# Kernel optimization log

Hardware: AMD Instinct MI355X
Metric: run time of the kernel (lower is better)

## Reference

```python
import jax, jax.numpy as jnp
import numpy as np

N_APP = 100000
N_ATTR = 50000
E = 500000
D_IN = 128
D_H = 128
D_OUT = 2


def _sage(h_src, h_dst, src, dst, ew, W_self, W_neigh, b, n_dst):
    # DGL SAGEConv('mean') with edge_weight: m_e = ew_e * h_src[src_e];
    # h_neigh_v = sum_e->v m_e / in_degree(v); out = h_dst@W_self + h_neigh@W_neigh + b
    # (feat_drop=0.2 is identity in eval mode)
    m = h_src[src] * ew[:, None]                                   # [E, d]
    s = jax.ops.segment_sum(m, dst, num_segments=n_dst)            # [n_dst, d]
    deg = jax.ops.segment_sum(jnp.ones_like(ew), dst, num_segments=n_dst)
    h_neigh = s / jnp.maximum(deg, 1.0)[:, None]
    return h_dst @ W_self + h_neigh @ W_neigh + b


def _forward(x_app, x_attr, ew0, ew1, ew2,
             Wself1, Wneigh1, b1, Wself2, Wneigh2, b2, Wc, bc,
             src0, dst0, src1, dst1, src2, dst2):
    # ---- layer 1 (HeteroGraphConv, aggregate='sum' over relations per dst ntype) ----
    h_attr = _sage(x_app, x_attr, src0, dst0, ew0, Wself1[0], Wneigh1[0], b1[0], N_ATTR)
    h_app = (_sage(x_attr, x_app, src1, dst1, ew1, Wself1[1], Wneigh1[1], b1[1], N_APP)
             + _sage(x_app, x_app, src2, dst2, ew2, Wself1[2], Wneigh1[2], b1[2], N_APP))
    h_attr = jax.nn.relu(h_attr)
    h_app = jax.nn.relu(h_app)
    # ---- layer 2 ----
    h_attr2 = _sage(h_app, h_attr, src0, dst0, ew0, Wself2[0], Wneigh2[0], b2[0], N_ATTR)
    h_app2 = (_sage(h_attr, h_app, src1, dst1, ew1, Wself2[1], Wneigh2[1], b2[1], N_APP)
              + _sage(h_app, h_app, src2, dst2, ew2, Wself2[2], Wneigh2[2], b2[2], N_APP))
    del h_attr2  # second layer output on 'attribute' is unused by classify
    # ---- classify on 'application' ----
    return h_app2 @ Wc + bc


def setup_inputs() -> dict:
    key = jax.random.key(0)
    ks = jax.random.split(key, 20)
    sc = 1.0 / np.sqrt(D_H)
    return {
        "x_app": jax.random.normal(ks[0], (N_APP, D_IN), jnp.float32),
        "x_attr": jax.random.normal(ks[1], (N_ATTR, D_IN), jnp.float32),
        "ew0": jax.random.uniform(ks[2], (E,), jnp.float32),
        "ew1": jax.random.uniform(ks[3], (E,), jnp.float32),
        "ew2": jax.random.uniform(ks[4], (E,), jnp.float32),
        "Wself1": jax.random.normal(ks[5], (3, D_IN, D_H), jnp.float32) * sc,
        "Wneigh1": jax.random.normal(ks[6], (3, D_IN, D_H), jnp.float32) * sc,
        "b1": jax.random.normal(ks[7], (3, D_H), jnp.float32) * 0.01,
        "Wself2": jax.random.normal(ks[8], (3, D_H, D_H), jnp.float32) * sc,
        "Wneigh2": jax.random.normal(ks[9], (3, D_H, D_H), jnp.float32) * sc,
        "b2": jax.random.normal(ks[10], (3, D_H), jnp.float32) * 0.01,
        "Wc": jax.random.normal(ks[11], (D_H, D_OUT), jnp.float32) * sc,
        "bc": jax.random.normal(ks[12], (D_OUT,), jnp.float32) * 0.01,
        "src0": jax.random.randint(ks[13], (E,), 0, N_APP, jnp.int32),
        "dst0": jax.random.randint(ks[14], (E,), 0, N_ATTR, jnp.int32),
        "src1": jax.random.randint(ks[15], (E,), 0, N_ATTR, jnp.int32),
        "dst1": jax.random.randint(ks[16], (E,), 0, N_APP, jnp.int32),
        "src2": jax.random.randint(ks[17], (E,), 0, N_APP, jnp.int32),
        "dst2": jax.random.randint(ks[18], (E,), 0, N_APP, jnp.int32),
    }


def reference(x_app, x_attr, ew0, ew1, ew2,
              Wself1, Wneigh1, b1, Wself2, Wneigh2, b2, Wc, bc,
              src0, dst0, src1, dst1, src2, dst2):
    return _forward(x_app, x_attr, ew0, ew1, ew2,
                    Wself1, Wneigh1, b1, Wself2, Wneigh2, b2, Wc, bc,
                    src0, dst0, src1, dst1, src2, dst2)
```

## Files before the change

kernel.cpp:

```cpp
#include <hip/hip_runtime.h>

#define NAPP  100000
#define NATTR 50000
#define NE    500000
#define D     128
#define NTOT  (NATTR + 2 * NAPP)
#define SCHUNK 1024
#define SNB   ((NTOT + SCHUNK - 1) / SCHUNK)
#define EGRID ((NE + 255) / 256)
#define GB_APP  ((NAPP + 63) / 64)
#define GB_ATTR ((NATTR + 63) / 64)

typedef __attribute__((ext_vector_type(8))) short bfrag;
typedef __attribute__((ext_vector_type(4))) float f32x4;

__device__ __forceinline__ short bf16_rn(float x) {
    union { float f; unsigned u; } a; a.f = x;
    unsigned r = (a.u + 0x7fffu + ((a.u >> 16) & 1u)) >> 16;
    return (short)r;
}
__device__ __forceinline__ float bf16_to_f(short s) {
    union { float f; unsigned u; } a;
    a.u = ((unsigned)(unsigned short)s) << 16;
    return a.f;
}

__device__ __forceinline__ void split2(float x, float y, unsigned& hw, unsigned& lw) {
    union { float f; unsigned u; } ax, ay;
    ax.f = x; ay.f = y;
    unsigned hx = (ax.u + 0x7fffu + ((ax.u >> 16) & 1u)) >> 16;
    unsigned hy = (ay.u + 0x7fffu + ((ay.u >> 16) & 1u)) >> 16;
    union { unsigned u; float f; } fx, fy;
    fx.u = hx << 16; fy.u = hy << 16;
    union { float f; unsigned u; } rx, ry;
    rx.f = x - fx.f; ry.f = y - fy.f;
    unsigned lx = (rx.u + 0x7fffu + ((rx.u >> 16) & 1u)) >> 16;
    unsigned ly = (ry.u + 0x7fffu + ((ry.u >> 16) & 1u)) >> 16;
    hw = (hy << 16) | (hx & 0xffffu);
    lw = (ly << 16) | (lx & 0xffffu);
}

__global__ __launch_bounds__(256) void hist3_kernel(
        const int* __restrict__ d0, const int* __restrict__ d1, const int* __restrict__ d2,
        int* __restrict__ h0, int* __restrict__ h1, int* __restrict__ h2) {
    int b = blockIdx.x;
    int rel = b / EGRID;
    int i = (b - rel * EGRID) * 256 + threadIdx.x;
    if (i >= NE) return;
    const int* dst = (rel == 0) ? d0 : (rel == 1) ? d1 : d2;
    int* h = (rel == 0) ? h0 : (rel == 1) ? h1 : h2;
    atomicAdd(&h[dst[i]], 1);
}

__global__ __launch_bounds__(256) void scan_partial_kernel(const int* __restrict__ cur,
                                                           int* __restrict__ bsum) {
    int b = blockIdx.x, t = threadIdx.x;
    int4 v = *((const int4*)(cur + b * SCHUNK) + t);
    int s = v.x + v.y + v.z + v.w;
    __shared__ int sd[256];
    sd[t] = s;
    __syncthreads();
    for (int off = 128; off > 0; off >>= 1) {
        if (t < off) sd[t] += sd[t + off];
        __syncthreads();
    }
    if (t == 0) bsum[b] = sd[0];
}

__global__ __launch_bounds__(256) void scan_offsets_kernel(const int* __restrict__ bsum,
        int* __restrict__ boff, int* __restrict__ rp0, int* __restrict__ rp1,
        int* __restrict__ rp2) {
    int t = threadIdx.x;
    int v = (t < SNB) ? bsum[t] : 0;
    __shared__ int sd[256];
    sd[t] = v;
    __syncthreads();
    for (int off = 1; off < 256; off <<= 1) {
        int u = (t >= off) ? sd[t - off] : 0;
        __syncthreads();
        sd[t] += u;
        __syncthreads();
    }
    boff[t] = sd[t] - v;
    if (t == 0) { rp0[NATTR] = NE; rp1[NAPP] = NE; rp2[NAPP] = NE; }
}

__global__ __launch_bounds__(256) void scan_final_kernel(int* __restrict__ cur,
        const int* __restrict__ boff, int* __restrict__ rp0, int* __restrict__ rp1,
        int* __restrict__ rp2) {
    int b = blockIdx.x, t = threadIdx.x;
    int base = b * SCHUNK + t * 4;
    int4 v = *(const int4*)(cur + base);
    int s = v.x + v.y + v.z + v.w;
    __shared__ int sd[256];
    sd[t] = s;
    __syncthreads();
    for (int off = 1; off < 256; off <<= 1) {
        int u = (t >= off) ? sd[t - off] : 0;
        __syncthreads();
        sd[t] += u;
        __syncthreads();
    }
    int pre = boff[b] + sd[t] - s;
    int ex[4];
    ex[0] = pre;
    ex[1] = ex[0] + v.x;
    ex[2] = ex[1] + v.y;
    ex[3] = ex[2] + v.z;
    #pragma unroll
    for (int i = 0; i < 4; i++) {
        int idx = base + i;
        if (idx < NTOT) {
            int* rp; int loc; int rbase;
            if (idx < NATTR)             { rp = rp0; loc = idx;                 rbase = 0; }
            else if (idx < NATTR + NAPP) { rp = rp1; loc = idx - NATTR;        rbase = NE; }
            else                         { rp = rp2; loc = idx - NATTR - NAPP; rbase = 2 * NE; }
            int val = ex[i] - rbase;
            rp[loc] = val;
            cur[idx] = val;
        }
    }
}

__global__ __launch_bounds__(256) void scatter3_kernel(
        const int* __restrict__ s0, const int* __restrict__ d0, const float* __restrict__ e0,
        int* __restrict__ c0, int2* __restrict__ cw0,
        const int* __restrict__ s1, const int* __restrict__ d1, const float* __restrict__ e1,
        int* __restrict__ c1, int2* __restrict__ cw1,
        const int* __restrict__ s2, const int* __restrict__ d2, const float* __restrict__ e2,
        int* __restrict__ c2, int2* __restrict__ cw2) {
    int b = blockIdx.x;
    int rel = b / EGRID;
    int i = (b - rel * EGRID) * 256 + threadIdx.x;
    if (i >= NE) return;
    const int* src; const int* dst; const float* ew; int* cur; int2* cw;
    if (rel == 0)      { src = s0; dst = d0; ew = e0; cur = c0; cw = cw0; }
    else if (rel == 1) { src = s1; dst = d1; ew = e1; cur = c1; cw = cw1; }
    else               { src = s2; dst = d2; ew = e2; cur = c2; cw = cw2; }
    int p = atomicAdd(&cur[dst[i]], 1);
    int2 v;
    v.x = src[i];
    v.y = __float_as_int(ew[i]);
    cw[p] = v;
}

__global__ __launch_bounds__(256) void pack_kernel(
        const float* __restrict__ Wself1, const float* __restrict__ Wneigh1,
        const float* __restrict__ Wself2, const float* __restrict__ Wneigh2,
        const float* __restrict__ b1, const float* __restrict__ b2,
        const float* __restrict__ Wc, const float* __restrict__ bc,
        short* __restrict__ PBh, short* __restrict__ PBl,
        float* __restrict__ b1s, float* __restrict__ b2s,
        float* __restrict__ Cs, float* __restrict__ C1, float* __restrict__ C2,
        float* __restrict__ bconst) {
    int m = blockIdx.x;
    if (m == 8) {
        int tid = threadIdx.x;
        int k = tid >> 1, j = tid & 1;
        const float* Wn1 = Wneigh2 + D * D;
        const float* Wn2 = Wneigh2 + 2 * D * D;
        const float* Ws1 = Wself2 + D * D;
        const float* Ws2 = Wself2 + 2 * D * D;
        float ss = 0.f, s1 = 0.f, s2 = 0.f;
        for (int tt = 0; tt < D; tt++) {
            float wc = Wc[tt * 2 + j];
            ss += (Ws1[k * D + tt] + Ws2[k * D + tt]) * wc;
            s1 += Wn1[k * D + tt] * wc;
            s2 += Wn2[k * D + tt] * wc;
        }
        Cs[tid] = ss; C1[tid] = s1; C2[tid] = s2;
        if (tid < 2) {
            float s = bc[tid];
            for (int tt = 0; tt < D; tt++)
                s += (b2[D + tt] + b2[2 * D + tt]) * Wc[tt * 2 + tid];
            bconst[tid] = s;
        }
        return;
    }
    const float* srcA; const float* srcB = nullptr;
    switch (m) {
        case 0: srcA = Wself1; break;
        case 1: srcA = Wneigh1; break;
        case 2: srcA = Wself1 + D * D; srcB = Wself1 + 2 * D * D; break;
        case 3: srcA = Wneigh1 + D * D; break;
        case 4: srcA = Wneigh1 + 2 * D * D; break;
        case 5: srcA = Wself2 + D * D; srcB = Wself2 + 2 * D * D; break;
        case 6: srcA = Wneigh2 + D * D; break;
        default: srcA = Wneigh2 + 2 * D * D; break;
    }
    short* oh = PBh + (size_t)m * D * D;
    short* ol = PBl + (size_t)m * D * D;
    for (int i = threadIdx.x; i < D * D; i += 256) {
        int k = i >> 7, n = i & 127;
        float v = srcA[i];
        if (srcB) v += srcB[i];
        short hi = bf16_rn(v);
        short lo = bf16_rn(v - bf16_to_f(hi));
        int kc = k >> 5, q = (k >> 3) & 3, j = k & 7, nt = n >> 4, c = n & 15;
        int pos = (((kc * 8 + nt) * 64) + q * 16 + c) * 8 + j;
        oh[pos] = hi;
        ol[pos] = lo;
    }
    if (m == 0 && threadIdx.x < D) {
        int t = threadIdx.x;
        b1s[t] = b1[D + t] + b1[2 * D + t];
        b2s[t] = b2[D + t] + b2[2 * D + t];
    }
}

#define ASTR 128
template<int NG>
__device__ __forceinline__ void fused_body(
        const float* __restrict__ in0, const short* __restrict__ B0h, const short* __restrict__ B0l,
        const float* __restrict__ x1, const int* __restrict__ rp1, const int2* __restrict__ cw1,
        const short* __restrict__ B1h, const short* __restrict__ B1l,
        const float* __restrict__ x2, const int* __restrict__ rp2, const int2* __restrict__ cw2,
        const short* __restrict__ B2h, const short* __restrict__ B2l,
        const float* __restrict__ bias,
        const float* __restrict__ Ccol0, const float* __restrict__ Ccol1,
        float* __restrict__ zo0, float* __restrict__ zo1,
        int nrows, int row0, float* At) {
    const int t = threadIdx.x;
    const int w = t >> 6, lane = t & 63;
    const int q = lane >> 4, c = lane & 15;
    const int myrow = row0 + w * 16 + c;
    const int arow = min(myrow, nrows - 1);

    f32x4 acc[8];
    #pragma unroll
    for (int nt = 0; nt < 8; nt++) acc[nt] = (f32x4){0.f, 0.f, 0.f, 0.f};

    {
        const float* __restrict__ arp = in0 + (size_t)arow * D;
        const bfrag* __restrict__ Bh = (const bfrag*)B0h;
        const bfrag* __restrict__ Bl = (const bfrag*)B0l;
        #pragma unroll
        for (int kc = 0; kc < 4; kc++) {
            float4 a0 = *(const float4*)(arp + kc * 32 + q * 8);
            float4 a1 = *(const float4*)(arp + kc * 32 + q * 8 + 4);
            union { unsigned u[4]; bfrag v; } ahu, alu;
            split2(a0.x, a0.y, ahu.u[0], alu.u[0]);
            split2(a0.z, a0.w, ahu.u[1], alu.u[1]);
            split2(a1.x, a1.y, ahu.u[2], alu.u[2]);
            split2(a1.z, a1.w, ahu.u[3], alu.u[3]);
            bfrag ah = ahu.v, al = alu.v;
            const bfrag* bh = Bh + kc * 512 + lane;
            const bfrag* bl = Bl + kc * 512 + lane;
            #pragma unroll
            for (int nt = 0; nt < 8; nt++) {
                bfrag vh = bh[nt * 64];
                bfrag vl = bl[nt * 64];
                acc[nt] = __builtin_amdgcn_mfma_f32_16x16x32_bf16(ah, vh, acc[nt], 0, 0, 0);
                acc[nt] = __builtin_amdgcn_mfma_f32_16x16x32_bf16(ah, vl, acc[nt], 0, 0, 0);
                acc[nt] = __builtin_amdgcn_mfma_f32_16x16x32_bf16(al, vh, acc[nt], 0, 0, 0);
            }
        }
    }

    const int grp = t >> 5, l32 = t & 31;
    #pragma unroll
    for (int g = 0; g < NG; g++) {
        const float* __restrict__ xs = (g == 0) ? x1 : x2;
        const int* __restrict__ rp   = (g == 0) ? rp1 : rp2;
        const int2* __restrict__ cw  = (g == 0) ? cw1 : cw2;
        const short* __restrict__ Bhp = (g == 0) ? B1h : B2h;
        const short* __restrict__ Blp = (g == 0) ? B1l : B2l;

        if (g > 0) __syncthreads();
        {
            const int r0g = row0 + grp * 8;
            int bnd[9];
            #pragma unroll
            for (int i = 0; i < 9; i++) bnd[i] = rp[min(r0g + i, nrows)];
            #pragma unroll
            for (int p = 0; p < 4; p++) {
                const int A0 = bnd[2 * p],     A1 = bnd[2 * p + 1];
                const int B0 = bnd[2 * p + 1], B1 = bnd[2 * p + 2];
                float4 aA = make_float4(0.f, 0.f, 0.f, 0.f);
                float4 aB = make_float4(0.f, 0.f, 0.f, 0.f);
                const int lastA = min(max(A1 - 1, A0), NE - 1);
                const int lastB = min(max(B1 - 1, B0), NE - 1);
                int jA = A0, jB = B0;
                while (jA < A1 || jB < B1) {
                    int2 ed[8];
                    #pragma unroll
                    for (int u = 0; u < 4; u++) ed[u] = cw[min(jA + u, lastA)];
                    #pragma unroll
                    for (int u = 0; u < 4; u++) ed[4 + u] = cw[min(jB + u, lastB)];
                    float wt[8];
                    #pragma unroll
                    for (int u = 0; u < 4; u++)
                        wt[u] = (jA + u < A1) ? __int_as_float(ed[u].y) : 0.f;
                    #pragma unroll
                    for (int u = 0; u < 4; u++)
                        wt[4 + u] = (jB + u < B1) ? __int_as_float(ed[4 + u].y) : 0.f;
                    float4 v[8];
                    #pragma unroll
                    for (int u = 0; u < 8; u++)
                        v[u] = *(const float4*)(xs + (size_t)ed[u].x * D + l32 * 4);
                    aA.x += wt[0] * v[0].x + wt[1] * v[1].x + wt[2] * v[2].x + wt[3] * v[3].x;
                    aA.y += wt[0] * v[0].y + wt[1] * v[1].y + wt[2] * v[2].y + wt[3] * v[3].y;
                    aA.z += wt[0] * v[0].z + wt[1] * v[1].z + wt[2] * v[2].z + wt[3] * v[3].z;
                    aA.w += wt[0] * v[0].w + wt[1] * v[1].w + wt[2] * v[2].w + wt[3] * v[3].w;
                    aB.x += wt[4] * v[4].x + wt[5] * v[5].x + wt[6] * v[6].x + wt[7] * v[7].x;
                    aB.y += wt[4] * v[4].y + wt[5] * v[5].y + wt[6] * v[6].y + wt[7] * v[7].y;
                    aB.z += wt[4] * v[4].z + wt[5] * v[5].z + wt[6] * v[6].z + wt[7] * v[7].z;
                    aB.w += wt[4] * v[4].w + wt[5] * v[5].w + wt[6] * v[6].w + wt[7] * v[7].w;
                    jA += 4; jB += 4;
                }
                const float invA = 1.0f / (float)max(A1 - A0, 1);
                const float invB = 1.0f / (float)max(B1 - B0, 1);
                aA.x *= invA; aA.y *= invA; aA.z *= invA; aA.w *= invA;
                aB.x *= invB; aB.y *= invB; aB.z *= invB; aB.w *= invB;
                const int lrA = grp * 8 + 2 * p;
                const int lrB = lrA + 1;
                *(float4*)&At[lrA * ASTR + ((l32 ^ ((lrA & 3) << 1)) << 2)] = aA;
                *(float4*)&At[lrB * ASTR + ((l32 ^ ((lrB & 3) << 1)) << 2)] = aB;
            }
        }
        __syncthreads();

        const bfrag* __restrict__ Bh = (const bfrag*)Bhp;
        const bfrag* __restrict__ Bl = (const bfrag*)Blp;
        const int rloc = w * 16 + c;
        const int sw = (rloc & 3) << 1;
        const float* __restrict__ arow_lds = &At[rloc * ASTR];
        #pragma unroll
        for (int kc = 0; kc < 4; kc++) {
            const int g0 = kc * 8 + q * 2;
            float4 a0 = *(const float4*)(arow_lds + ((g0 ^ sw) << 2));
            float4 a1 = *(const float4*)(arow_lds + (((g0 + 1) ^ sw) << 2));
            union { unsigned u[4]; bfrag v; } ahu, alu;
            split2(a0.x, a0.y, ahu.u[0], alu.u[0]);
            split2(a0.z, a0.w, ahu.u[1], alu.u[1]);
            split2(a1.x, a1.y, ahu.u[2], alu.u[2]);
            split2(a1.z, a1.w, ahu.u[3], alu.u[3]);
            bfrag ah = ahu.v, al = alu.v;
            const bfrag* bh = Bh + kc * 512 + lane;
            const bfrag* bl = Bl + kc * 512 + lane;
            #pragma unroll
            for (int nt = 0; nt < 8; nt++) {
                bfrag vh = bh[nt * 64];
                bfrag vl = bl[nt * 64];
                acc[nt] = __builtin_amdgcn_mfma_f32_16x16x32_bf16(ah, vh, acc[nt], 0, 0, 0);
                acc[nt] = __builtin_amdgcn_mfma_f32_16x16x32_bf16(ah, vl, acc[nt], 0, 0, 0);
                acc[nt] = __builtin_amdgcn_mfma_f32_16x16x32_bf16(al, vh, acc[nt], 0, 0, 0);
            }
        }
    }

    float c00[8], c01[8], c10[8], c11[8], bvv[8];
    #pragma unroll
    for (int nt = 0; nt < 8; nt++) {
        float2 v0 = *(const float2*)(Ccol0 + (nt * 16 + c) * 2);
        c00[nt] = v0.x; c01[nt] = v0.y;
        if (NG == 2) {
            float2 v1 = *(const float2*)(Ccol1 + (nt * 16 + c) * 2);
            c10[nt] = v1.x; c11[nt] = v1.y;
        }
        bvv[nt] = bias[nt * 16 + c];
    }
    #pragma unroll
    for (int r = 0; r < 4; r++) {
        int row = row0 + w * 16 + q * 4 + r;
        float s0 = 0.f, s1 = 0.f, t0 = 0.f, t1 = 0.f;
        #pragma unroll
        for (int nt = 0; nt < 8; nt++) {
            float h = fmaxf(acc[nt][r] + bvv[nt], 0.f);
            s0 += h * c00[nt]; s1 += h * c01[nt];
            if (NG == 2) { t0 += h * c10[nt]; t1 += h * c11[nt]; }
        }
        #pragma unroll
        for (int off = 1; off < 16; off <<= 1) {
            s0 += __shfl_xor(s0, off);
            s1 += __shfl_xor(s1, off);
            if (NG == 2) { t0 += __shfl_xor(t0, off); t1 += __shfl_xor(t1, off); }
        }
        if (c == 0 && row < nrows) {
            *(float2*)(zo0 + (size_t)row * 2) = make_float2(s0, s1);
            if (NG == 2) *(float2*)(zo1 + (size_t)row * 2) = make_float2(t0, t1);
        }
    }
}

__global__ __launch_bounds__(256, 4) void fused_all_kernel(
        const float* __restrict__ xapp, const float* __restrict__ xattr,
        const short* __restrict__ PBh, const short* __restrict__ PBl,
        const int* __restrict__ rp0, const int2* __restrict__ cw0,
        const int* __restrict__ rp1, const int2* __restrict__ cw1,
        const int* __restrict__ rp2, const int2* __restrict__ cw2,
        const float* __restrict__ b1, const float* __restrict__ b1s,
        const float* __restrict__ Cs, const float* __restrict__ C2,
        const float* __restrict__ C1,
        float* __restrict__ zs, float* __restrict__ z2, float* __restrict__ za) {
    __shared__ __align__(16) float At[64 * ASTR];
    const size_t MM = (size_t)D * D;
    int b = blockIdx.x;
    if (b < GB_APP) {
        fused_body<2>(xapp, PBh + 2 * MM, PBl + 2 * MM,
                      xattr, rp1, cw1, PBh + 3 * MM, PBl + 3 * MM,
                      xapp,  rp2, cw2, PBh + 4 * MM, PBl + 4 * MM,
                      b1s, Cs, C2, zs, z2, NAPP, b * 64, At);
    } else {
        int bb = b - GB_APP;
        fused_body<1>(xattr, PBh, PBl,
                      xapp, rp0, cw0, PBh + 1 * MM, PBl + 1 * MM,
                      nullptr, nullptr, nullptr, nullptr, nullptr,
                      b1, C1, nullptr, za, nullptr, NATTR, bb * 64, At);
    }
}

__global__ __launch_bounds__(256) void final_out_kernel(
        const float* __restrict__ zs, const float* __restrict__ za,
        const float* __restrict__ z2,
        const int* __restrict__ rp1, const int2* __restrict__ cw1,
        const int* __restrict__ rp2, const int2* __restrict__ cw2,
        const float* __restrict__ bconst, float* __restrict__ out, int n) {
    int r = (blockIdx.x * 256 + threadIdx.x) >> 3;
    int l = threadIdx.x & 7;
    if (r >= n) return;
    int s0 = rp1[r], s1 = rp1[r + 1];
    float q0 = 0.f, q1 = 0.f;
    for (int j = s0 + l; j < s1; j += 8) {
        int2 e = cw1[j];
        float w = __int_as_float(e.y);
        float2 v = *(const float2*)(za + (size_t)e.x * 2);
        q0 += w * v.x; q1 += w * v.y;
    }
    float inv1 = 1.0f / (float)max(s1 - s0, 1);
    float p0 = q0 * inv1, p1 = q1 * inv1;
    s0 = rp2[r]; s1 = rp2[r + 1];
    q0 = 0.f; q1 = 0.f;
    for (int j = s0 + l; j < s1; j += 8) {
        int2 e = cw2[j];
        float w = __int_as_float(e.y);
        float2 v = *(const float2*)(z2 + (size_t)e.x * 2);
        q0 += w * v.x; q1 += w * v.y;
    }
    float inv2 = 1.0f / (float)max(s1 - s0, 1);
    p0 += q0 * inv2; p1 += q1 * inv2;
    #pragma unroll
    for (int off = 1; off < 8; off <<= 1) {
        p0 += __shfl_xor(p0, off);
        p1 += __shfl_xor(p1, off);
    }
    if (l == 0) {
        float2 s = *(const float2*)(zs + (size_t)r * 2);
        out[(size_t)r * 2 + 0] = p0 + s.x + bconst[0];
        out[(size_t)r * 2 + 1] = p1 + s.y + bconst[1];
    }
}

extern "C" void kernel_launch(void* const* d_in, const int* in_sizes, int n_in,
                              void* d_out, int out_size, void* d_ws, size_t ws_size,
                              hipStream_t stream) {
    const float* x_app   = (const float*)d_in[0];
    const float* x_attr  = (const float*)d_in[1];
    const float* ew0     = (const float*)d_in[2];
    const float* ew1     = (const float*)d_in[3];
    const float* ew2     = (const float*)d_in[4];
    const float* Wself1  = (const float*)d_in[5];
    const float* Wneigh1 = (const float*)d_in[6];
    const float* b1      = (const float*)d_in[7];
    const float* Wself2  = (const float*)d_in[8];
    const float* Wneigh2 = (const float*)d_in[9];
    const float* b2      = (const float*)d_in[10];
    const float* Wc      = (const float*)d_in[11];
    const float* bc      = (const float*)d_in[12];
    const int* src0 = (const int*)d_in[13];
    const int* dst0 = (const int*)d_in[14];
    const int* src1 = (const int*)d_in[15];
    const int* dst1 = (const int*)d_in[16];
    const int* src2 = (const int*)d_in[17];
    const int* dst2 = (const int*)d_in[18];
    float* out = (float*)d_out;

    float* ws = (float*)d_ws;
    float* h_attr = ws;
    float* h_app  = h_attr + (size_t)NATTR * D;
    float* b1s    = h_app  + (size_t)NAPP * D;
    float* b2s    = b1s + D;
    float* za     = b2s + D;
    float* zsv    = za + (size_t)NATTR * 2;
    float* z2v    = zsv + (size_t)NAPP * 2;
    float* Cs     = z2v + (size_t)NAPP * 2;
    float* C1     = Cs + 256;
    float* C2     = C1 + 256;
    float* bconst = C2 + 256;
    int* cur  = (int*)(bconst + 4);
    int* cur0 = cur;
    int* cur1 = cur0 + NATTR;
    int* cur2 = cur1 + NAPP;
    int* rp0  = cur + SNB * SCHUNK;
    int* rp1  = rp0 + NATTR + 4;
    int* rp2  = rp1 + NAPP + 4;
    int* bsum = rp2 + NAPP + 4;
    int* boff = bsum + 256;
    int2* cw0 = (int2*)(boff + 256);
    int2* cw1 = cw0 + NE;
    int2* cw2 = cw1 + NE;
    short* PBh = (short*)(cw2 + NE);
    short* PBl = PBh + (size_t)8 * D * D;

    hipMemsetAsync(cur, 0, (size_t)SNB * SCHUNK * sizeof(int), stream);

    pack_kernel<<<9, 256, 0, stream>>>(Wself1, Wneigh1, Wself2, Wneigh2,
                                       b1, b2, Wc, bc, PBh, PBl, b1s, b2s,
                                       Cs, C1, C2, bconst);

    hist3_kernel<<<3 * EGRID, 256, 0, stream>>>(dst0, dst1, dst2, cur0, cur1, cur2);
    scan_partial_kernel<<<SNB, 256, 0, stream>>>(cur, bsum);
    scan_offsets_kernel<<<1, 256, 0, stream>>>(bsum, boff, rp0, rp1, rp2);
    scan_final_kernel<<<SNB, 256, 0, stream>>>(cur, boff, rp0, rp1, rp2);
    scatter3_kernel<<<3 * EGRID, 256, 0, stream>>>(
        src0, dst0, ew0, cur0, cw0,
        src1, dst1, ew1, cur1, cw1,
        src2, dst2, ew2, cur2, cw2);

    fused_all_kernel<<<GB_APP + GB_ATTR, 256, 0, stream>>>(
        x_app, x_attr, PBh, PBl,
        rp0, cw0, rp1, cw1, rp2, cw2,
        b1, b1s, Cs, C2, C1, zsv, z2v, za);

    final_out_kernel<<<((size_t)NAPP * 8 + 255) / 256, 256, 0, stream>>>(
        zsv, za, z2v, rp1, cw1, rp2, cw2, bconst, out, NAPP);
}
```

Measured before the change: 502.4 us.

## Merge CSR build into one cooperative kernel and widen gather to four rows

Replaces the memset, pack, histogram, three scan kernels and the scatter kernel with a single cooperative kernel that uses grid-wide syncs between phases, removing several launch gaps. Separately, the neighbor aggregation loop now walks four destination rows at once instead of two, issuing 16 independent feature gathers per iteration to raise memory-level parallelism. The cooperative grid of 1024 blocks must be fully co-resident, and grid.sync adds its own barrier cost. The wider gather raises register pressure, which may lower occupancy.

After: 1.422 ms. 2.83x slower.

```diff
diff --git a/kernel.cpp b/kernel.cpp
--- a/kernel.cpp
+++ b/kernel.cpp
@@ -1,4 +1,7 @@
 #include <hip/hip_runtime.h>
+#include <hip/hip_cooperative_groups.h>
+
+namespace cg = cooperative_groups;
 
 #define NAPP  100000
 #define NATTR 50000
@@ -7,9 +10,9 @@
 #define NTOT  (NATTR + 2 * NAPP)
 #define SCHUNK 1024
 #define SNB   ((NTOT + SCHUNK - 1) / SCHUNK)
-#define EGRID ((NE + 255) / 256)
 #define GB_APP  ((NAPP + 63) / 64)
 #define GB_ATTR ((NATTR + 63) / 64)
+#define BUILD_GRID 1024
 
 typedef __attribute__((ext_vector_type(8))) short bfrag;
 typedef __attribute__((ext_vector_type(4))) float f32x4;
@@ -40,175 +43,185 @@
     lw = (ly << 16) | (lx & 0xffffu);
 }
 
-__global__ __launch_bounds__(256) void hist3_kernel(
-        const int* __restrict__ d0, const int* __restrict__ d1, const int* __restrict__ d2,
-        int* __restrict__ h0, int* __restrict__ h1, int* __restrict__ h2) {
-    int b = blockIdx.x;
-    int rel = b / EGRID;
-    int i = (b - rel * EGRID) * 256 + threadIdx.x;
-    if (i >= NE) return;
-    const int* dst = (rel == 0) ? d0 : (rel == 1) ? d1 : d2;
-    int* h = (rel == 0) ? h0 : (rel == 1) ? h1 : h2;
-    atomicAdd(&h[dst[i]], 1);
-}
-
-__global__ __launch_bounds__(256) void scan_partial_kernel(const int* __restrict__ cur,
-                                                           int* __restrict__ bsum) {
-    int b = blockIdx.x, t = threadIdx.x;
-    int4 v = *((const int4*)(cur + b * SCHUNK) + t);
-    int s = v.x + v.y + v.z + v.w;
+struct BuildArgs {
+    const int *s0, *d0; const float* e0;
+    const int *s1, *d1; const float* e1;
+    const int *s2, *d2; const float* e2;
+    const float *Wself1, *Wneigh1, *Wself2, *Wneigh2, *b1, *b2, *Wc, *bc;
+    short *PBh, *PBl;
+    float *b1s, *b2s, *Cs, *C1, *C2, *bconst;
+    int *cur, *rp0, *rp1, *rp2, *bsum, *boff;
+    int2 *cw0, *cw1, *cw2;
+};
+
+__global__ __launch_bounds__(256) void build_all_kernel(BuildArgs a) {
+    cg::grid_group grid = cg::this_grid();
     __shared__ int sd[256];
-    sd[t] = s;
-    __syncthreads();
-    for (int off = 128; off > 0; off >>= 1) {
-        if (t < off) sd[t] += sd[t + off];
+    const int t = threadIdx.x;
+    const int gtid = blockIdx.x * 256 + t;
+    const int gstride = BUILD_GRID * 256;
+    int* cur0 = a.cur;
+    int* cur1 = cur0 + NATTR;
+    int* cur2 = cur1 + NAPP;
+
+    if (blockIdx.x < 9) {
+        int m = blockIdx.x;
+        if (m == 8) {
+            int k = t >> 1, j = t & 1;
+            const float* Wn1 = a.Wneigh2 + D * D;
+            const float* Wn2 = a.Wneigh2 + 2 * D * D;
+            const float* Ws1 = a.Wself2 + D * D;
+            const float* Ws2 = a.Wself2 + 2 * D * D;
+            float ss = 0.f, s1 = 0.f, s2 = 0.f;
+            for (int tt = 0; tt < D; tt++) {
+                float wc = a.Wc[tt * 2 + j];
+                ss += (Ws1[k * D + tt] + Ws2[k * D + tt]) * wc;
+                s1 += Wn1[k * D + tt] * wc;
+                s2 += Wn2[k * D + tt] * wc;
+            }
+            a.Cs[t] = ss; a.C1[t] = s1; a.C2[t] = s2;
+            if (t < 2) {
+                float s = a.bc[t];
+                for (int tt = 0; tt < D; tt++)
+                    s += (a.b2[D + tt] + a.b2[2 * D + tt]) * a.Wc[tt * 2 + t];
+                a.bconst[t] = s;
+            }
+        } else {
+            const float* srcA; const float* srcB = nullptr;
+            switch (m) {
+                case 0: srcA = a.Wself1; break;
+                case 1: srcA = a.Wneigh1; break;
+                case 2: srcA = a.Wself1 + D * D; srcB = a.Wself1 + 2 * D * D; break;
+                case 3: srcA = a.Wneigh1 + D * D; break;
+                case 4: srcA = a.Wneigh1 + 2 * D * D; break;
+                case 5: srcA = a.Wself2 + D * D; srcB = a.Wself2 + 2 * D * D; break;
+                case 6: srcA = a.Wneigh2 + D * D; break;
+                default: srcA = a.Wneigh2 + 2 * D * D; break;
+            }
+            short* oh = a.PBh + (size_t)m * D * D;
+            short* ol = a.PBl + (size_t)m * D * D;
+            for (int i = t; i < D * D; i += 256) {
+                int k = i >> 7, n = i & 127;
+                float v = srcA[i];
+                if (srcB) v += srcB[i];
+                short hi = bf16_rn(v);
+                short lo = bf16_rn(v - bf16_to_f(hi));
+                int kc = k >> 5, q = (k >> 3) & 3, j = k & 7, nt = n >> 4, c = n & 15;
+                int pos = (((kc * 8 + nt) * 64) + q * 16 + c) * 8 + j;
+                oh[pos] = hi;
+                ol[pos] = lo;
+            }
+            if (m == 0 && t < D) {
+                a.b1s[t] = a.b1[D + t] + a.b1[2 * D + t];
+                a.b2s[t] = a.b2[D + t] + a.b2[2 * D + t];
+            }
+        }
+    } else {
+        int idx = (blockIdx.x - 9) * 256 + t;
+        const int n4 = (SNB * SCHUNK) / 4;
+        for (int i = idx; i < n4; i += (BUILD_GRID - 9) * 256)
+            *(int4*)(a.cur + i * 4) = make_int4(0, 0, 0, 0);
+    }
+    __threadfence();
+    grid.sync();
+
+    for (int i = gtid; i < NE; i += gstride) atomicAdd(&cur0[a.d0[i]], 1);
+    for (int i = gtid; i < NE; i += gstride) atomicAdd(&cur1[a.d1[i]], 1);
+    for (int i = gtid; i < NE; i += gstride) atomicAdd(&cur2[a.d2[i]], 1);
+    __threadfence();
+    grid.sync();
+
+    if (blockIdx.x < SNB) {
+        int b = blockIdx.x;
+        int4 v = *((const int4*)(a.cur + b * SCHUNK) + t);
+        int s = v.x + v.y + v.z + v.w;
+        sd[t] = s;
         __syncthreads();
-    }
-    if (t == 0) bsum[b] = sd[0];
-}
-
-__global__ __launch_bounds__(256) void scan_offsets_kernel(const int* __restrict__ bsum,
-        int* __restrict__ boff, int* __restrict__ rp0, int* __restrict__ rp1,
-        int* __restrict__ rp2) {
-    int t = threadIdx.x;
-    int v = (t < SNB) ? bsum[t] : 0;
-    __shared__ int sd[256];
-    sd[t] = v;
-    __syncthreads();
-    for (int off = 1; off < 256; off <<= 1) {
-        int u = (t >= off) ? sd[t - off] : 0;
+        for (int off = 128; off > 0; off >>= 1) {
+            if (t < off) sd[t] += sd[t + off];
+            __syncthreads();
+        }
+        if (t == 0) a.bsum[b] = sd[0];
+    }
+    __threadfence();
+    grid.sync();
+
+    if (blockIdx.x == 0) {
+        int v = (t < SNB) ? a.bsum[t] : 0;
+        sd[t] = v;
         __syncthreads();
-        sd[t] += u;
+        for (int off = 1; off < 256; off <<= 1) {
+            int u = (t >= off) ? sd[t - off] : 0;
+            __syncthreads();
+            sd[t] += u;
+            __syncthreads();
+        }
+        a.boff[t] = sd[t] - v;
+        if (t == 0) { a.rp0[NATTR] = NE; a.rp1[NAPP] = NE; a.rp2[NAPP] = NE; }
+    }
+    __threadfence();
+    grid.sync();
+
+    if (blockIdx.x < SNB) {
+        int b = blockIdx.x;
+        int base = b * SCHUNK + t * 4;
+        int4 v = *(const int4*)(a.cur + base);
+        int s = v.x + v.y + v.z + v.w;
+        sd[t] = s;
         __syncthreads();
-    }
-    boff[t] = sd[t] - v;
-    if (t == 0) { rp0[NATTR] = NE; rp1[NAPP] = NE; rp2[NAPP] = NE; }
-}
-
-__global__ __launch_bounds__(256) void scan_final_kernel(int* __restrict__ cur,
-        const int* __restrict__ boff, int* __restrict__ rp0, int* __restrict__ rp1,
-        int* __restrict__ rp2) {
-    int b = blockIdx.x, t = threadIdx.x;
-    int base = b * SCHUNK + t * 4;
-    int4 v = *(const int4*)(cur + base);
-    int s = v.x + v.y + v.z + v.w;
-    __shared__ int sd[256];
-    sd[t] = s;
-    __syncthreads();
-    for (int off = 1; off < 256; off <<= 1) {
-        int u = (t >= off) ? sd[t - off] : 0;
-        __syncthreads();
-        sd[t] += u;
-        __syncthreads();
-    }
-    int pre = boff[b] + sd[t] - s;
-    int ex[4];
-    ex[0] = pre;
-    ex[1] = ex[0] + v.x;
-    ex[2] = ex[1] + v.y;
-    ex[3] = ex[2] + v.z;
-    #pragma unroll
-    for (int i = 0; i < 4; i++) {
-        int idx = base + i;
-        if (idx < NTOT) {
-            int* rp; int loc; int rbase;
-            if (idx < NATTR)             { rp = rp0; loc = idx;                 rbase = 0; }
-            else if (idx < NATTR + NAPP) { rp = rp1; loc = idx - NATTR;        rbase = NE; }
-            else                         { rp = rp2; loc = idx - NATTR - NAPP; rbase = 2 * NE; }
-            int val = ex[i] - rbase;
-            rp[loc] = val;
-            cur[idx] = val;
-        }
-    }
-}
-
-__global__ __launch_bounds__(256) void scatter3_kernel(
-        const int* __restrict__ s0, const int* __restrict__ d0, const float* __restrict__ e0,
-        int* __restrict__ c0, int2* __restrict__ cw0,
-        const int* __restrict__ s1, const int* __restrict__ d1, const float* __restrict__ e1,
-        int* __restrict__ c1, int2* __restrict__ cw1,
-        const int* __restrict__ s2, const int* __restrict__ d2, const float* __restrict__ e2,
-        int* __restrict__ c2, int2* __restrict__ cw2) {
-    int b = blockIdx.x;
-    int rel = b / EGRID;
-    int i = (b - rel * EGRID) * 256 + threadIdx.x;
-    if (i >= NE) return;
-    const int* src; const int* dst; const float* ew; int* cur; int2* cw;
-    if (rel == 0)      { src = s0; dst = d0; ew = e0; cur = c0; cw = cw0; }
-    else if (rel == 1) { src = s1; dst = d1; ew = e1; cur = c1; cw = cw1; }
-    else               { src = s2; dst = d2; ew = e2; cur = c2; cw = cw2; }
-    int p = atomicAdd(&cur[dst[i]], 1);
-    int2 v;
-    v.x = src[i];
-    v.y = __float_as_int(ew[i]);
-    cw[p] = v;
-}
-
-__global__ __launch_bounds__(256) void pack_kernel(
-        const float* __restrict__ Wself1, const float* __restrict__ Wneigh1,
-        const float* __restrict__ Wself2, const float* __restrict__ Wneigh2,
-        const float* __restrict__ b1, const float* __restrict__ b2,
-        const float* __restrict__ Wc, const float* __restrict__ bc,
-        short* __restrict__ PBh, short* __restrict__ PBl,
-        float* __restrict__ b1s, float* __restrict__ b2s,
-        float* __restrict__ Cs, float* __restrict__ C1, float* __restrict__ C2,
-        float* __restrict__ bconst) {
-    int m = blockIdx.x;
-    if (m == 8) {
-        int tid = threadIdx.x;
-        int k = tid >> 1, j = tid & 1;
-        const float* Wn1 = Wneigh2 + D * D;
-        const float* Wn2 = Wneigh2 + 2 * D * D;
-        const float* Ws1 = Wself2 + D * D;
-        const float* Ws2 = Wself2 + 2 * D * D;
-        float ss = 0.f, s1 = 0.f, s2 = 0.f;
-        for (int tt = 0; tt < D; tt++) {
-            float wc = Wc[tt * 2 + j];
-            ss += (Ws1[k * D + tt] + Ws2[k * D + tt]) * wc;
-            s1 += Wn1[k * D + tt] * wc;
-            s2 += Wn2[k * D + tt] * wc;
-        }
-        Cs[tid] = ss; C1[tid] = s1; C2[tid] = s2;
-        if (tid < 2) {
-            float s = bc[tid];
-            for (int tt = 0; tt < D; tt++)
-                s += (b2[D + tt] + b2[2 * D + tt]) * Wc[tt * 2 + tid];
-            bconst[tid] = s;
-        }
-        return;
-    }
-    const float* srcA; const float* srcB = nullptr;
-    switch (m) {
-        case 0: srcA = Wself1; break;
-        case 1: srcA = Wneigh1; break;
-        case 2: srcA = Wself1 + D * D; srcB = Wself1 + 2 * D * D; break;
-        case 3: srcA = Wneigh1 + D * D; break;
-        case 4: srcA = Wneigh1 + 2 * D * D; break;
-        case 5: srcA = Wself2 + D * D; srcB = Wself2 + 2 * D * D; break;
-        case 6: srcA = Wneigh2 + D * D; break;
-        default: srcA = Wneigh2 + 2 * D * D; break;
-    }
-    short* oh = PBh + (size_t)m * D * D;
-    short* ol = PBl + (size_t)m * D * D;
-    for (int i = threadIdx.x; i < D * D; i += 256) {
-        int k = i >> 7, n = i & 127;
-        float v = srcA[i];
-        if (srcB) v += srcB[i];
-        short hi = bf16_rn(v);
-        short lo = bf16_rn(v - bf16_to_f(hi));
-        int kc = k >> 5, q = (k >> 3) & 3, j = k & 7, nt = n >> 4, c = n & 15;
-        int pos = (((kc * 8 + nt) * 64) + q * 16 + c) * 8 + j;
-        oh[pos] = hi;
-        ol[pos] = lo;
-    }
-    if (m == 0 && threadIdx.x < D) {
-        int t = threadIdx.x;
-        b1s[t] = b1[D + t] + b1[2 * D + t];
-        b2s[t] = b2[D + t] + b2[2 * D + t];
+        for (int off = 1; off < 256; off <<= 1) {
+            int u = (t >= off) ? sd[t - off] : 0;
+            __syncthreads();
+            sd[t] += u;
+            __syncthreads();
+        }
+        int pre = a.boff[b] + sd[t] - s;
+        int ex[4];
+        ex[0] = pre;
+        ex[1] = ex[0] + v.x;
+        ex[2] = ex[1] + v.y;
+        ex[3] = ex[2] + v.z;
+        #pragma unroll
+        for (int i = 0; i < 4; i++) {
+            int idx = base + i;
+            if (idx < NTOT) {
+                int* rp; int loc; int rbase;
+                if (idx < NATTR)             { rp = a.rp0; loc = idx;                 rbase = 0; }
+                else if (idx < NATTR + NAPP) { rp = a.rp1; loc = idx - NATTR;        rbase = NE; }
+                else                         { rp = a.rp2; loc = idx - NATTR - NAPP; rbase = 2 * NE; }
+                int val = ex[i] - rbase;
+                rp[loc] = val;
+                a.cur[idx] = val;
+            }
+        }
+    }
+    __threadfence();
+    grid.sync();
+
+    for (int i = gtid; i < NE; i += gstride) {
+        int p = atomicAdd(&cur0[a.d0[i]], 1);
+        int2 v; v.x = a.s0[i]; v.y = __float_as_int(a.e0[i]);
+        a.cw0[p] = v;
+    }
+    for (int i = gtid; i < NE; i += gstride) {
+        int p = atomicAdd(&cur1[a.d1[i]], 1);
+        int2 v; v.x = a.s1[i]; v.y = __float_as_int(a.e1[i]);
+        a.cw1[p] = v;
+    }
+    for (int i = gtid; i < NE; i += gstride) {
+        int p = atomicAdd(&cur2[a.d2[i]], 1);
+        int2 v; v.x = a.s2[i]; v.y = __float_as_int(a.e2[i]);
+        a.cw2[p] = v;
     }
 }
 
 #define ASTR 128
+#define ACC4(dst, b) \
+    dst.x += wt[b] * v[b].x + wt[b+1] * v[b+1].x + wt[b+2] * v[b+2].x + wt[b+3] * v[b+3].x; \
+    dst.y += wt[b] * v[b].y + wt[b+1] * v[b+1].y + wt[b+2] * v[b+2].y + wt[b+3] * v[b+3].y; \
+    dst.z += wt[b] * v[b].z + wt[b+1] * v[b+1].z + wt[b+2] * v[b+2].z + wt[b+3] * v[b+3].z; \
+    dst.w += wt[b] * v[b].w + wt[b+1] * v[b+1].w + wt[b+2] * v[b+2].w + wt[b+3] * v[b+3].w;
+
 template<int NG>
 __device__ __forceinline__ void fused_body(
         const float* __restrict__ in0, const short* __restrict__ B0h, const short* __restrict__ B0l,
@@ -273,49 +286,60 @@
             #pragma unroll
             for (int i = 0; i < 9; i++) bnd[i] = rp[min(r0g + i, nrows)];
             #pragma unroll
-            for (int p = 0; p < 4; p++) {
-                const int A0 = bnd[2 * p],     A1 = bnd[2 * p + 1];
-                const int B0 = bnd[2 * p + 1], B1 = bnd[2 * p + 2];
+            for (int p = 0; p < 2; p++) {
+                const int rb0 = bnd[4 * p],     rb1 = bnd[4 * p + 1];
+                const int rb2 = bnd[4 * p + 2], rb3 = bnd[4 * p + 3];
+                const int rb4 = bnd[4 * p + 4];
                 float4 aA = make_float4(0.f, 0.f, 0.f, 0.f);
                 float4 aB = make_float4(0.f, 0.f, 0.f, 0.f);
-                const int lastA = min(max(A1 - 1, A0), NE - 1);
-                const int lastB = min(max(B1 - 1, B0), NE - 1);
-                int jA = A0, jB = B0;
-                while (jA < A1 || jB < B1) {
-                    int2 ed[8];
+                float4 aC = make_float4(0.f, 0.f, 0.f, 0.f);
+                float4 aD = make_float4(0.f, 0.f, 0.f, 0.f);
+                const int lA = min(max(rb1 - 1, rb0), NE - 1);
+                const int lB = min(max(rb2 - 1, rb1), NE - 1);
+                const int lC = min(max(rb3 - 1, rb2), NE - 1);
+                const int lD = min(max(rb4 - 1, rb3), NE - 1);
+                int jA = rb0, jB = rb1, jC = rb2, jD = rb3;
+                while (jA < rb1 || jB < rb2 || jC < rb3 || jD < rb4) {
+                    int2 ed[16];
                     #pragma unroll
-                    for (int u = 0; u < 4; u++) ed[u] = cw[min(jA + u, lastA)];
+                    for (int u = 0; u < 4; u++) ed[u]      = cw[min(jA + u, lA)];
                     #pragma unroll
-                    for (int u = 0; u < 4; u++) ed[4 + u] = cw[min(jB + u, lastB)];
-                    float wt[8];
+                    for (int u = 0; u < 4; u++) ed[4 + u]  = cw[min(jB + u, lB)];
                     #pragma unroll
-                    for (int u = 0; u < 4; u++)
-                        wt[u] = (jA + u < A1) ? __int_as_float(ed[u].y) : 0.f;
+                    for (int u = 0; u < 4; u++) ed[8 + u]  = cw[min(jC + u, lC)];
                     #pragma unroll
-                    for (int u = 0; u < 4; u++)
-                        wt[4 + u] = (jB + u < B1) ? __int_as_float(ed[4 + u].y) : 0.f;
-                    float4 v[8];
+                    for (int u = 0; u < 4; u++) ed[12 + u] = cw[min(jD + u, lD)];
+                    float wt[16];
                     #pragma unroll
-                    for (int u = 0; u < 8; u++)
+                    for (int u = 0; u < 4; u++) {
+                        wt[u]      = (jA + u < rb1) ? __int_as_float(ed[u].y)      : 0.f;
+                        wt[4 + u]  = (jB + u < rb2) ? __int_as_float(ed[4 + u].y)  : 0.f;
+                        wt[8 + u]  = (jC + u < rb3) ? __int_as_float(ed[8 + u].y)  : 0.f;
+                        wt[12 + u] = (jD + u < rb4) ? __int_as_float(ed[12 + u].y) : 0.f;
+                    }
+                    float4 v[16];
+                    #pragma unroll
+                    for (int u = 0; u < 16; u++)
                         v[u] = *(const float4*)(xs + (size_t)ed[u].x * D + l32 * 4);
-                    aA.x += wt[0] * v[0].x + wt[1] * v[1].x + wt[2] * v[2].x + wt[3] * v[3].x;
-                    aA.y += wt[0] * v[0].y + wt[1] * v[1].y + wt[2] * v[2].y + wt[3] * v[3].y;
-                    aA.z += wt[0] * v[0].z + wt[1] * v[1].z + wt[2] * v[2].z + wt[3] * v[3].z;
-                    aA.w += wt[0] * v[0].w + wt[1] * v[1].w + wt[2] * v[2].w + wt[3] * v[3].w;
-                    aB.x += wt[4] * v[4].x + wt[5] * v[5].x + wt[6] * v[6].x + wt[7] * v[7].x;
-                    aB.y += wt[4] * v[4].y + wt[5] * v[5].y + wt[6] * v[6].y + wt[7] * v[7].y;
-                    aB.z += wt[4] * v[4].z + wt[5] * v[5].z + wt[6] * v[6].z + wt[7] * v[7].z;
-                    aB.w += wt[4] * v[4].w + wt[5] * v[5].w + wt[6] * v[6].w + wt[7] * v[7].w;
-                    jA += 4; jB += 4;
+                    ACC4(aA, 0)
+                    ACC4(aB, 4)
+                    ACC4(aC, 8)
+                    ACC4(aD, 12)
+                    jA += 4; jB += 4; jC += 4; jD += 4;
                 }
-                const float invA = 1.0f / (float)max(A1 - A0, 1);
-                const float invB = 1.0f / (float)max(B1 - B0, 1);
+                const float invA = 1.0f / (float)max(rb1 - rb0, 1);
+                const float invB = 1.0f / (float)max(rb2 - rb1, 1);
+                const float invC = 1.0f / (float)max(rb3 - rb2, 1);
+                const float invD = 1.0f / (float)max(rb4 - rb3, 1);
                 aA.x *= invA; aA.y *= invA; aA.z *= invA; aA.w *= invA;
                 aB.x *= invB; aB.y *= invB; aB.z *= invB; aB.w *= invB;
-                const int lrA = grp * 8 + 2 * p;
-                const int lrB = lrA + 1;
-                *(float4*)&At[lrA * ASTR + ((l32 ^ ((lrA & 3) << 1)) << 2)] = aA;
-                *(float4*)&At[lrB * ASTR + ((l32 ^ ((lrB & 3) << 1)) << 2)] = aB;
+                aC.x *= invC; aC.y *= invC; aC.z *= invC; aC.w *= invC;
+                aD.x *= invD; aD.y *= invD; aD.z *= invD; aD.w *= invD;
+                const int lr0 = grp * 8 + 4 * p;
+                *(float4*)&At[(lr0 + 0) * ASTR + ((l32 ^ (((lr0 + 0) & 3) << 1)) << 2)] = aA;
+                *(float4*)&At[(lr0 + 1) * ASTR + ((l32 ^ (((lr0 + 1) & 3) << 1)) << 2)] = aB;
+                *(float4*)&At[(lr0 + 2) * ASTR + ((l32 ^ (((lr0 + 2) & 3) << 1)) << 2)] = aC;
+                *(float4*)&At[(lr0 + 3) * ASTR + ((l32 ^ (((lr0 + 3) & 3) << 1)) << 2)] = aD;
             }
         }
         __syncthreads();
@@ -488,9 +512,6 @@
     float* C2     = C1 + 256;
     float* bconst = C2 + 256;
     int* cur  = (int*)(bconst + 4);
-    int* cur0 = cur;
-    int* cur1 = cur0 + NATTR;
-    int* cur2 = cur1 + NAPP;
     int* rp0  = cur + SNB * SCHUNK;
     int* rp1  = rp0 + NATTR + 4;
     int* rp2  = rp1 + NAPP + 4;
@@ -502,20 +523,19 @@
     short* PBh = (short*)(cw2 + NE);
     short* PBl = PBh + (size_t)8 * D * D;
 
-    hipMemsetAsync(cur, 0, (size_t)SNB * SCHUNK * sizeof(int), stream);
-
-    pack_kernel<<<9, 256, 0, stream>>>(Wself1, Wneigh1, Wself2, Wneigh2,
-                                       b1, b2, Wc, bc, PBh, PBl, b1s, b2s,
-                                       Cs, C1, C2, bconst);
-
-    hist3_kernel<<<3 * EGRID, 256, 0, stream>>>(dst0, dst1, dst2, cur0, cur1, cur2);
-    scan_partial_kernel<<<SNB, 256, 0, stream>>>(cur, bsum);
-    scan_offsets_kernel<<<1, 256, 0, stream>>>(bsum, boff, rp0, rp1, rp2);
-    scan_final_kernel<<<SNB, 256, 0, stream>>>(cur, boff, rp0, rp1, rp2);
-    scatter3_kernel<<<3 * EGRID, 256, 0, stream>>>(
-        src0, dst0, ew0, cur0, cw0,
-        src1, dst1, ew1, cur1, cw1,
-        src2, dst2, ew2, cur2, cw2);
+    BuildArgs ba;
+    ba.s0 = src0; ba.d0 = dst0; ba.e0 = ew0;
+    ba.s1 = src1; ba.d1 = dst1; ba.e1 = ew1;
+    ba.s2 = src2; ba.d2 = dst2; ba.e2 = ew2;
+    ba.Wself1 = Wself1; ba.Wneigh1 = Wneigh1; ba.Wself2 = Wself2; ba.Wneigh2 = Wneigh2;
+    ba.b1 = b1; ba.b2 = b2; ba.Wc = Wc; ba.bc = bc;
+    ba.PBh = PBh; ba.PBl = PBl;
+    ba.b1s = b1s; ba.b2s = b2s; ba.Cs = Cs; ba.C1 = C1; ba.C2 = C2; ba.bconst = bconst;
+    ba.cur = cur; ba.rp0 = rp0; ba.rp1 = rp1; ba.rp2 = rp2; ba.bsum = bsum; ba.boff = boff;
+    ba.cw0 = cw0; ba.cw1 = cw1; ba.cw2 = cw2;
+    void* kargs[] = { (void*)&ba };
+    hipLaunchCooperativeKernel(reinterpret_cast<void*>(build_all_kernel),
+                               dim3(BUILD_GRID), dim3(256), kargs, 0, stream);
 
     fused_all_kernel<<<GB_APP + GB_ATTR, 256, 0, stream>>>(
         x_app, x_attr, PBh, PBl,
```
